# Kernel optimization log

Hardware: AMD Instinct MI355X
Metric: run time of the kernel (lower is better)

The kernel has to match this reference:

```python
import jax, jax.numpy as jnp
import numpy as np

IMG = 1024.0
POOL = 7
STRIDES = (4, 8, 16, 32)  # levels P2..P5
STDS = jnp.array([0.1, 0.1, 0.2, 0.2], dtype=jnp.float32)  # RCNN_TARGET_STDS


def delta2bbox(rois, deltas):
    # rois: [N,4] (y1,x1,y2,x2) pixels; deltas: [N,4]
    d = deltas * STDS  # means are zero
    y1, x1, y2, x2 = rois[:, 0], rois[:, 1], rois[:, 2], rois[:, 3]
    h = y2 - y1
    w = x2 - x1
    cy = y1 + 0.5 * h + d[:, 0] * h
    cx = x1 + 0.5 * w + d[:, 1] * w
    h = h * jnp.exp(d[:, 2])
    w = w * jnp.exp(d[:, 3])
    b = jnp.stack([cy - 0.5 * h, cx - 0.5 * w, cy + 0.5 * h, cx + 0.5 * w], axis=1)
    return jnp.clip(b, 0.0, IMG)


def crop_level(feat, rois, stride):
    # feat: [H,W,C]; bilinear 7x7 crop (crop_and_resize style)
    H, W, _ = feat.shape
    s = rois / stride
    grid = (jnp.arange(POOL, dtype=jnp.float32) + 0.5) / POOL
    ys = s[:, 0:1] + grid[None, :] * (s[:, 2:3] - s[:, 0:1])  # [N,7]
    xs = s[:, 1:2] + grid[None, :] * (s[:, 3:4] - s[:, 1:2])  # [N,7]
    y0f = jnp.clip(jnp.floor(ys), 0.0, H - 1)
    x0f = jnp.clip(jnp.floor(xs), 0.0, W - 1)
    y0 = y0f.astype(jnp.int32)
    x0 = x0f.astype(jnp.int32)
    y1 = jnp.minimum(y0 + 1, H - 1)
    x1 = jnp.minimum(x0 + 1, W - 1)
    wy = jnp.clip(ys - y0f, 0.0, 1.0)[:, :, None, None]  # [N,7,1,1]
    wx = jnp.clip(xs - x0f, 0.0, 1.0)[:, None, :, None]  # [N,1,7,1]
    g = lambda yi, xi: feat[yi[:, :, None], xi[:, None, :]]  # [N,7,7,C]
    return (g(y0, x0) * (1 - wy) * (1 - wx) + g(y0, x1) * (1 - wy) * wx
            + g(y1, x0) * wy * (1 - wx) + g(y1, x1) * wy * wx)


def pyramid_roi_align(feats, rois):
    h = rois[:, 2] - rois[:, 0]
    w = rois[:, 3] - rois[:, 1]
    lvl = jnp.floor(4.0 + jnp.log2(jnp.sqrt(jnp.maximum(h * w, 1e-6)) / 224.0))
    lvl = jnp.clip(lvl, 2.0, 5.0).astype(jnp.int32)
    pooled = 0.0
    for i, (feat, stride) in enumerate(zip(feats, STRIDES)):
        mask = (lvl == i + 2).astype(feat.dtype)[:, None, None, None]
        pooled = pooled + crop_level(feat, rois, stride) * mask
    return pooled  # [N,7,7,C]


def bbox_head(pooled, i, fc1_w, fc1_b, fc2_w, fc2_b, cls_w, cls_b, reg_w, reg_b):
    n = pooled.shape[0]
    x = pooled.reshape(n, -1)
    h1 = jax.nn.relu(x @ fc1_w[i] + fc1_b[i])
    h2 = jax.nn.relu(h1 @ fc2_w[i] + fc2_b[i])
    logits = h2 @ cls_w[i] + cls_b[i]
    probs = jax.nn.softmax(logits, axis=-1)
    deltas = h2 @ reg_w[i] + reg_b[i]
    return logits, probs, deltas


def setup_inputs() -> dict:
    key = jax.random.key(0)
    ks = jax.random.split(key, 16)
    d = {}
    for j, (name, shp) in enumerate([("P2", (1, 256, 256, 256)), ("P3", (1, 128, 128, 256)),
                                     ("P4", (1, 64, 64, 256)), ("P5", (1, 32, 32, 256))]):
        d[name] = jax.random.normal(ks[j], shp, dtype=jnp.float32)
    N = 1000
    u = jax.random.uniform(ks[4], (N, 4))
    hh = 16.0 * 2.0 ** (u[:, 0] * 5.0)  # box sizes 16..512 px, spans all pyramid levels
    ww = 16.0 * 2.0 ** (u[:, 1] * 5.0)
    y1 = u[:, 2] * (IMG - hh)
    x1 = u[:, 3] * (IMG - ww)
    d["rois"] = jnp.stack([y1, x1, y1 + hh, x1 + ww], axis=1)
    d["fc1_w"] = jax.random.normal(ks[5], (3, 12544, 1024), dtype=jnp.float32) * 0.01
    d["fc1_b"] = jnp.zeros((3, 1024), jnp.float32)
    d["fc2_w"] = jax.random.normal(ks[6], (3, 1024, 1024), dtype=jnp.float32) * 0.02
    d["fc2_b"] = jnp.zeros((3, 1024), jnp.float32)
    d["cls_w"] = jax.random.normal(ks[7], (3, 1024, 81), dtype=jnp.float32) * 0.02
    d["cls_b"] = jnp.zeros((3, 81), jnp.float32)
    d["reg_w"] = jax.random.normal(ks[8], (3, 1024, 4), dtype=jnp.float32) * 0.01
    d["reg_b"] = jnp.zeros((3, 4), jnp.float32)
    return d


def reference(P2, P3, P4, P5, rois, fc1_w, fc1_b, fc2_w, fc2_b, cls_w, cls_b, reg_w, reg_b):
    feats = [P2[0], P3[0], P4[0], P5[0]]
    params = (fc1_w, fc1_b, fc2_w, fc2_b, cls_w, cls_b, reg_w, reg_b)
    r = rois
    probs3 = None
    pooled = None
    for i in range(3):
        pooled = pyramid_roi_align(feats, r)
        _, probs3, deltas = bbox_head(pooled, i, *params)
        if i < 2:
            r = delta2bbox(r, deltas)
    # test-time ensemble: heads 1 and 2 re-applied to final pooled regions
    _, probs1, _ = bbox_head(pooled, 0, *params)
    _, probs2, _ = bbox_head(pooled, 1, *params)
    return (probs3 + probs1 + probs2) / 3.0
```

## Files before the change

kernel.cpp:

```cpp
#include <hip/hip_runtime.h>


#define BM 128
#define BN 128
#define BK 32
#define K1 12544
#define MPAD 1024
#define NROI 1000

typedef __bf16 bf16_t;
typedef bf16_t bf16x8 __attribute__((ext_vector_type(8)));
typedef float f32x4 __attribute__((ext_vector_type(4)));
typedef float f32x2 __attribute__((ext_vector_type(2)));
typedef unsigned short u16x4 __attribute__((ext_vector_type(4)));
typedef unsigned short u16x2 __attribute__((ext_vector_type(2)));

__device__ __forceinline__ unsigned short f2bf(float x) {
  unsigned u = __float_as_uint(x);
  return (unsigned short)((u + 0x7fffu + ((u >> 16) & 1u)) >> 16);
}
__device__ __forceinline__ float bf2f(unsigned short h) {
  return __uint_as_float(((unsigned)h) << 16);
}

__device__ __forceinline__ void gld_lds16(const void* g, void* l) {
  __builtin_amdgcn_global_load_lds(
      (__attribute__((address_space(1))) void*)g,
      (__attribute__((address_space(3))) void*)l, 16, 0, 0);
}

template <bool SPLIT>
__global__ __launch_bounds__(256, 4)
void gemm_bf16(const unsigned short* __restrict__ Ah,
               const unsigned short* __restrict__ Al,
               long long strideA_head,
               const unsigned short* __restrict__ Bh,
               const unsigned short* __restrict__ Bl,
               long long strideB_head,
               float* __restrict__ Cpart,
               int Nh, int K, int kcSteps)
{
  __shared__ __align__(16) unsigned short sAh[BM * BK];
  __shared__ __align__(16) unsigned short sBh[BN * BK];
  __shared__ __align__(16) unsigned short sAl[SPLIT ? BM * BK : 8];
  __shared__ __align__(16) unsigned short sBl[SPLIT ? BN * BK : 8];

  const int t = threadIdx.x;
  const int ntile = Nh / BN;
  const int bm = blockIdx.x / ntile;
  const int bn = blockIdx.x % ntile;
  const int s = blockIdx.y;
  const int h = blockIdx.z;
  const int H = gridDim.z;

  const unsigned short* Ab = Ah + (size_t)h * strideA_head + (size_t)bm * BM * K;
  const unsigned short* Bb = Bh + (size_t)h * strideB_head + (size_t)bn * BN * K;
  const unsigned short* Alb = SPLIT ? (Al + (size_t)h * strideA_head + (size_t)bm * BM * K) : (const unsigned short*)0;
  const unsigned short* Blb = SPLIT ? (Bl + (size_t)h * strideB_head + (size_t)bn * BN * K) : (const unsigned short*)0;

  int k0 = s * kcSteps * BK;
  int k1 = min(K, k0 + kcSteps * BK);

  const int srow = t >> 2;
  const int gsw = ((t & 3) ^ ((srow >> 1) & 3)) * 8;
  const int lane = t & 63;
  const int wv = t >> 6;
  const int wm = (wv >> 1) * 64;
  const int wn = (wv & 1) * 64;
  const int lr = lane & 15;
  const int q = lane >> 4;
  const int sw = (lr >> 1) & 3;
  const int cA = (q ^ sw) * 8;

  f32x4 acc[4][4];
  const f32x4 z = {0.f, 0.f, 0.f, 0.f};
#pragma unroll
  for (int i = 0; i < 4; ++i)
#pragma unroll
    for (int j = 0; j < 4; ++j) acc[i][j] = z;

  for (int kk = k0; kk < k1; kk += BK) {
#pragma unroll
    for (int j = 0; j < 2; ++j) {
      int row = j * 64 + srow;
      gld_lds16(Ab + (size_t)row * K + kk + gsw, (char*)sAh + j * 4096 + t * 16);
      gld_lds16(Bb + (size_t)row * K + kk + gsw, (char*)sBh + j * 4096 + t * 16);
      if constexpr (SPLIT) {
        gld_lds16(Alb + (size_t)row * K + kk + gsw, (char*)sAl + j * 4096 + t * 16);
        gld_lds16(Blb + (size_t)row * K + kk + gsw, (char*)sBl + j * 4096 + t * 16);
      }
    }
    __syncthreads();

    bf16x8 af[4], bfr[4];
#pragma unroll
    for (int i = 0; i < 4; ++i) af[i] = *(const bf16x8*)&sAh[(wm + i * 16 + lr) * BK + cA];
#pragma unroll
    for (int j = 0; j < 4; ++j) bfr[j] = *(const bf16x8*)&sBh[(wn + j * 16 + lr) * BK + cA];
#pragma unroll
    for (int i = 0; i < 4; ++i)
#pragma unroll
      for (int j = 0; j < 4; ++j)
        acc[i][j] = __builtin_amdgcn_mfma_f32_16x16x32_bf16(af[i], bfr[j], acc[i][j], 0, 0, 0);

    if constexpr (SPLIT) {
      bf16x8 al[4], bl[4];
#pragma unroll
      for (int i = 0; i < 4; ++i) al[i] = *(const bf16x8*)&sAl[(wm + i * 16 + lr) * BK + cA];
#pragma unroll
      for (int j = 0; j < 4; ++j) bl[j] = *(const bf16x8*)&sBl[(wn + j * 16 + lr) * BK + cA];
#pragma unroll
      for (int i = 0; i < 4; ++i)
#pragma unroll
        for (int j = 0; j < 4; ++j) {
          acc[i][j] = __builtin_amdgcn_mfma_f32_16x16x32_bf16(af[i], bl[j], acc[i][j], 0, 0, 0);
          acc[i][j] = __builtin_amdgcn_mfma_f32_16x16x32_bf16(al[i], bfr[j], acc[i][j], 0, 0, 0);
        }
    }
    __syncthreads();
  }

  float* Cb = Cpart + ((size_t)(s * H + h) * MPAD + (size_t)bm * BM) * Nh + (size_t)bn * BN;
#pragma unroll
  for (int i = 0; i < 4; ++i)
#pragma unroll
    for (int j = 0; j < 4; ++j)
#pragma unroll
      for (int r = 0; r < 4; ++r) {
        int m = wm + i * 16 + q * 4 + r;
        int n = wn + j * 16 + lr;
        Cb[(size_t)m * Nh + n] = acc[i][j][r];
      }
}

#define DS_A(XB, MH) do { \
    rA[0][0]=lda_f(XB,(MH)*4+0,0); rA[0][1]=lda_f(XB,(MH)*4+0,1); \
    rA[1][0]=lda_f(XB,(MH)*4+1,0); rA[1][1]=lda_f(XB,(MH)*4+1,1); \
    rA[2][0]=lda_f(XB,(MH)*4+2,0); rA[2][1]=lda_f(XB,(MH)*4+2,1); \
    rA[3][0]=lda_f(XB,(MH)*4+3,0); rA[3][1]=lda_f(XB,(MH)*4+3,1); } while(0)

#define DS_B(XB, NH) do { \
    rB[(NH)*2+0][0]=ldb_f(XB,(NH)*2+0,0); rB[(NH)*2+0][1]=ldb_f(XB,(NH)*2+0,1); \
    rB[(NH)*2+1][0]=ldb_f(XB,(NH)*2+1,0); rB[(NH)*2+1][1]=ldb_f(XB,(NH)*2+1,1); } while(0)

#define MFMA_Q(MH, NH) do { \
  _Pragma("unroll") \
  for (int ii = 0; ii < 4; ++ii) { \
    _Pragma("unroll") \
    for (int jj = 0; jj < 2; ++jj) { \
      acc[(MH)*4+ii][(NH)*2+jj] = __builtin_amdgcn_mfma_f32_16x16x32_bf16(rA[ii][0], rB[(NH)*2+jj][0], acc[(MH)*4+ii][(NH)*2+jj], 0, 0, 0); \
      acc[(MH)*4+ii][(NH)*2+jj] = __builtin_amdgcn_mfma_f32_16x16x32_bf16(rA[ii][1], rB[(NH)*2+jj][1], acc[(MH)*4+ii][(NH)*2+jj], 0, 0, 0); \
    } } } while(0)

#define PHASE_SYNC() do { \
  __builtin_amdgcn_s_barrier(); \
  asm volatile("s_waitcnt lgkmcnt(0)" ::: "memory"); \
  __builtin_amdgcn_sched_barrier(0); } while(0)

#define PHASE_END() do { \
  __builtin_amdgcn_s_setprio(0); \
  __builtin_amdgcn_s_barrier(); } while(0)

__global__ __launch_bounds__(512, 2)
void gemm256_bf16(const unsigned short* __restrict__ A,
                  const unsigned short* __restrict__ B,
                  float* __restrict__ Cpart,
                  int Ntot, int K, int tilesTotal)
{
  extern __shared__ char lds[];
  const int t = threadIdx.x;
  const int ntile = Ntot >> 8;
  const int bm = blockIdx.x / ntile;
  const int bn = blockIdx.x % ntile;
  const int s = blockIdx.y;
  const int S = gridDim.y;
  const int qp = tilesTotal / S, rp = tilesTotal % S;
  const int t0 = s * qp + (s < rp ? s : rp);
  const int np = qp + (s < rp ? 1 : 0);

  const unsigned short* Ab = A + (size_t)bm * 256 * K;
  const unsigned short* Bb = B + (size_t)bn * 256 * K;

  const int srow = t >> 3;
  const int sgrp = ((t & 7) ^ (srow & 7)) << 3;

  const int lane = t & 63;
  const int wv = t >> 6;
  const int wm = (wv >> 2) << 7;
  const int wn = (wv & 3) << 6;
  const int lr = lane & 15;
  const int q = lane >> 4;

  f32x4 acc[8][4];
  const f32x4 z = {0.f, 0.f, 0.f, 0.f};
#pragma unroll
  for (int i = 0; i < 8; ++i)
#pragma unroll
    for (int j = 0; j < 4; ++j) acc[i][j] = z;

  bf16x8 rA[4][2], rB[4][2];

  auto stage_tile = [&](int xbuf, int kt) {
    const size_t col = ((size_t)(t0 + kt) << 6) + sgrp;
#pragma unroll
    for (int u = 0; u < 4; ++u) {
      const unsigned short* src = (u < 2) ? Ab : Bb;
      const int rbase = ((u & 1) << 7) + srow;
      char* dst = lds + xbuf * 65536 + ((u & 2) << 14) + ((u & 1) << 14) + t * 16;
      gld_lds16(src + (size_t)rbase * K + col, dst);
      gld_lds16(src + (size_t)(rbase + 64) * K + col, dst + 8192);
    }
  };

  auto lda_f = [&](int xbuf, int i, int ks) -> bf16x8 {
    const int row = wm + (i << 4) + lr;
    const int pg = (ks * 4 + q) ^ (row & 7);
    return *(const bf16x8*)(lds + xbuf * 65536 + row * 128 + pg * 16);
  };
  auto ldb_f = [&](int xbuf, int j, int ks) -> bf16x8 {
    const int row = wn + (j << 4) + lr;
    const int pg = (ks * 4 + q) ^ (row & 7);
    return *(const bf16x8*)(lds + xbuf * 65536 + 32768 + row * 128 + pg * 16);
  };

  stage_tile(0, 0);
  if (np > 1) {
    stage_tile(1, 1);
    asm volatile("s_waitcnt vmcnt(8)" ::: "memory");
  } else {
    asm volatile("s_waitcnt vmcnt(0)" ::: "memory");
  }
  __builtin_amdgcn_s_barrier();

  for (int i = 0; i < np; ++i) {
    const int buf = i & 1;
    const bool st = (i + 2 < np);
    DS_A(buf, 0);
    DS_B(buf, 0);
    PHASE_SYNC();
    __builtin_amdgcn_s_setprio(1);
    MFMA_Q(0, 0);
    PHASE_END();
    DS_B(buf, 1);
    PHASE_SYNC();
    __builtin_amdgcn_s_setprio(1);
    MFMA_Q(0, 1);
    PHASE_END();
    DS_A(buf, 1);
    PHASE_SYNC();
    __builtin_amdgcn_s_setprio(1);
    MFMA_Q(1, 0);
    PHASE_END();
    if (st) {
      stage_tile(buf, i + 2);
      asm volatile("s_waitcnt vmcnt(8)" ::: "memory");
    } else {
      asm volatile("s_waitcnt vmcnt(0)" ::: "memory");
    }
    __builtin_amdgcn_s_barrier();
    __builtin_amdgcn_sched_barrier(0);
    __builtin_amdgcn_s_setprio(1);
    MFMA_Q(1, 1);
    __builtin_amdgcn_s_setprio(0);
  }

  float* Cb = Cpart + (size_t)s * MPAD * Ntot +
              (size_t)(bm * 256 + wm) * Ntot + bn * 256 + wn;
#pragma unroll
  for (int i = 0; i < 8; ++i)
#pragma unroll
    for (int j = 0; j < 4; ++j)
#pragma unroll
      for (int r = 0; r < 4; ++r)
        Cb[(size_t)(i * 16 + q * 4 + r) * Ntot + j * 16 + lr] = acc[i][j][r];
}

__global__ __launch_bounds__(256)
void epilogue_kernel(const float* __restrict__ Cpart, int S, int H, int Nh,
                     const float* __restrict__ bias,
                     unsigned short* __restrict__ ohi,
                     unsigned short* __restrict__ olo, int flags)
{
  size_t total = (size_t)H * MPAD * Nh;
  size_t idx = ((size_t)blockIdx.x * 256 + threadIdx.x) * 4;
  if (idx >= total) return;
  int n = (int)(idx % Nh);
  int h = (int)(idx / ((size_t)MPAD * Nh));
  f32x4 v = *(const f32x4*)&bias[(size_t)h * Nh + n];
  for (int s = 0; s < S; ++s) v += *(const f32x4*)&Cpart[(size_t)s * total + idx];
  u16x4 hi, lo;
#pragma unroll
  for (int j = 0; j < 4; ++j) {
    float x = fmaxf(v[j], 0.f);
    hi[j] = f2bf(x);
    lo[j] = f2bf(x - bf2f(hi[j]));
  }
  *(u16x4*)&ohi[idx] = hi;
  if (flags & 4) *(u16x4*)&olo[idx] = lo;
}

__global__ __launch_bounds__(256)
void epilogue_fc1_s2(const float* __restrict__ Cpart, int S,
                     const float* __restrict__ bias,
                     unsigned short* __restrict__ ohi)
{
  const size_t total = (size_t)MPAD * 3072;
  size_t idx = ((size_t)blockIdx.x * 256 + threadIdx.x) * 4;
  if (idx >= total) return;
  int n = (int)(idx % 3072);
  int m = (int)(idx / 3072);
  f32x4 v = *(const f32x4*)&bias[n];
  for (int s = 0; s < S; ++s) v += *(const f32x4*)&Cpart[(size_t)s * total + idx];
  u16x4 hi;
#pragma unroll
  for (int j = 0; j < 4; ++j) hi[j] = f2bf(fmaxf(v[j], 0.f));
  int h = n >> 10;
  *(u16x4*)&ohi[((size_t)h * MPAD + m) * 1024 + (n & 1023)] = hi;
}

__global__ __launch_bounds__(256)
void transpose_convert(const float* __restrict__ W,
                       unsigned short* __restrict__ Thi,
                       unsigned short* __restrict__ Tlo,
                       int K, int N, int loHeads)
{
  __shared__ float tile[32][260];
  int kb = blockIdx.x * 256;
  int nb = blockIdx.y * 32;
  int h = blockIdx.z;
  const float* Wb = W + (size_t)h * K * N + (size_t)kb * N + nb;
  int tn = threadIdx.x & 31;
  int tk = threadIdx.x >> 5;
#pragma unroll
  for (int i = 0; i < 32; ++i) {
    int k = tk + i * 8;
    tile[tn][k] = Wb[(size_t)k * N + tn];
  }
  __syncthreads();
  bool wlo = h < loHeads;
  int l = threadIdx.x & 63;
  int ng = threadIdx.x >> 6;
  size_t ob = (size_t)h * N * K + (size_t)nb * K + kb;
#pragma unroll
  for (int i = 0; i < 8; ++i) {
    int n = ng + i * 4;
    f32x4 v = *(const f32x4*)&tile[n][4 * l];
    u16x4 hi;
#pragma unroll
    for (int j = 0; j < 4; ++j) hi[j] = f2bf(v[j]);
    *(u16x4*)&Thi[ob + (size_t)n * K + 4 * l] = hi;
    if (wlo) {
      u16x4 lo;
#pragma unroll
      for (int j = 0; j < 4; ++j) lo[j] = f2bf(v[j] - bf2f(hi[j]));
      *(u16x4*)&Tlo[ob + (size_t)n * K + 4 * l] = lo;
    }
  }
}

__global__ void transpose_cls(const float* __restrict__ W, unsigned short* __restrict__ T)
{
  int n = blockIdx.x, h = blockIdx.y, t = threadIdx.x;
  size_t ob = ((size_t)h * 128 + n) * 1024;
  if (n < 81) {
    for (int k = t; k < 1024; k += 256)
      T[ob + k] = f2bf(W[((size_t)h * 1024 + k) * 81 + n]);
  } else {
    for (int k = t; k < 1024; k += 256) T[ob + k] = 0;
  }
}

__global__ void roi_align_kernel(const float* __restrict__ rois,
                                 const float* __restrict__ P2, const float* __restrict__ P3,
                                 const float* __restrict__ P4, const float* __restrict__ P5,
                                 unsigned short* __restrict__ phi,
                                 unsigned short* __restrict__ plo, int writeLo)
{
  int m = blockIdx.x;
  int t = threadIdx.x;
  int c = (t & 63) * 4;
  int pg = t >> 6;
  const float* rp = rois + m * 4;
  float y1 = rp[0], x1 = rp[1], y2 = rp[2], x2 = rp[3];
  float hh = y2 - y1, ww = x2 - x1;
  float a = sqrtf(fmaxf(hh * ww, 1e-6f)) / 224.0f;
  float lvl = floorf(4.0f + log2f(a));
  lvl = fminf(fmaxf(lvl, 2.0f), 5.0f);
  int i = (int)lvl - 2;
  const float* f = (i == 0) ? P2 : (i == 1) ? P3 : (i == 2) ? P4 : P5;
  int H = 256 >> i;
  float stride = (float)(4 << i);
  float sy1 = y1 / stride, sx1 = x1 / stride;
  float dy = y2 / stride - sy1, dx = x2 / stride - sx1;
  size_t base = (size_t)m * K1 + c;
  for (int p = pg; p < 49; p += 4) {
    int py = p / 7, px = p % 7;
    float ys = sy1 + ((py + 0.5f) / 7.0f) * dy;
    float xs = sx1 + ((px + 0.5f) / 7.0f) * dx;
    float y0f = fminf(fmaxf(floorf(ys), 0.0f), (float)(H - 1));
    float x0f = fminf(fmaxf(floorf(xs), 0.0f), (float)(H - 1));
    int y0 = (int)y0f, x0 = (int)x0f;
    int y1i = min(y0 + 1, H - 1), x1i = min(x0 + 1, H - 1);
    float wy = fminf(fmaxf(ys - y0f, 0.0f), 1.0f);
    float wx = fminf(fmaxf(xs - x0f, 0.0f), 1.0f);
    f32x4 v00 = *(const f32x4*)(f + ((size_t)y0 * H + x0) * 256 + c);
    f32x4 v01 = *(const f32x4*)(f + ((size_t)y0 * H + x1i) * 256 + c);
    f32x4 v10 = *(const f32x4*)(f + ((size_t)y1i * H + x0) * 256 + c);
    f32x4 v11 = *(const f32x4*)(f + ((size_t)y1i * H + x1i) * 256 + c);
    float w00 = (1.f - wy) * (1.f - wx), w01 = (1.f - wy) * wx;
    float w10 = wy * (1.f - wx), w11 = wy * wx;
    f32x4 v = v00 * w00 + v01 * w01 + v10 * w10 + v11 * w11;
    u16x4 hi;
#pragma unroll
    for (int j = 0; j < 4; ++j) hi[j] = f2bf(v[j]);
    *(u16x4*)&phi[base + p * 256] = hi;
    if (writeLo) {
      u16x4 lo;
#pragma unroll
      for (int j = 0; j < 4; ++j) lo[j] = f2bf(v[j] - bf2f(hi[j]));
      *(u16x2*)&plo[base + p * 256] = *(u16x2*)&lo;
      *(u16x2*)&plo[base + p * 256 + 2] = *((u16x2*)&lo + 1);
    }
  }
}

__global__ void reg_delta_kernel(const float* __restrict__ Cpart, int S,
                                 const float* __restrict__ fb,
                                 const float* __restrict__ rw, const float* __restrict__ rb,
                                 const float* __restrict__ rin, float* __restrict__ rout)
{
  int m = blockIdx.x, t = threadIdx.x;
  float s0 = 0, s1 = 0, s2 = 0, s3 = 0;
  for (int n = t; n < 1024; n += 256) {
    float v = fb[n];
    for (int s = 0; s < S; ++s) v += Cpart[((size_t)s * 1024 + m) * 1024 + n];
    v = fmaxf(v, 0.f);
    const float* w = rw + (size_t)n * 4;
    s0 += v * w[0]; s1 += v * w[1]; s2 += v * w[2]; s3 += v * w[3];
  }
#pragma unroll
  for (int o = 32; o > 0; o >>= 1) {
    s0 += __shfl_xor(s0, o, 64);
    s1 += __shfl_xor(s1, o, 64);
    s2 += __shfl_xor(s2, o, 64);
    s3 += __shfl_xor(s3, o, 64);
  }
  __shared__ float part[4][4];
  int w = t >> 6;
  if ((t & 63) == 0) { part[w][0] = s0; part[w][1] = s1; part[w][2] = s2; part[w][3] = s3; }
  __syncthreads();
  if (t == 0) {
    float d0 = (part[0][0] + part[1][0] + part[2][0] + part[3][0] + rb[0]) * 0.1f;
    float d1 = (part[0][1] + part[1][1] + part[2][1] + part[3][1] + rb[1]) * 0.1f;
    float d2 = (part[0][2] + part[1][2] + part[2][2] + part[3][2] + rb[2]) * 0.2f;
    float d3 = (part[0][3] + part[1][3] + part[2][3] + part[3][3] + rb[3]) * 0.2f;
    const float* r = rin + m * 4;
    float y1 = r[0], x1 = r[1], y2 = r[2], x2 = r[3];
    float h = y2 - y1, wd = x2 - x1;
    float cy = y1 + 0.5f * h + d0 * h;
    float cx = x1 + 0.5f * wd + d1 * wd;
    float nh = h * expf(d2);
    float nw = wd * expf(d3);
    float* ro = rout + m * 4;
    ro[0] = fminf(fmaxf(cy - 0.5f * nh, 0.f), 1024.f);
    ro[1] = fminf(fmaxf(cx - 0.5f * nw, 0.f), 1024.f);
    ro[2] = fminf(fmaxf(cy + 0.5f * nh, 0.f), 1024.f);
    ro[3] = fminf(fmaxf(cx + 0.5f * nw, 0.f), 1024.f);
  }
}

__global__ void softmax_avg_kernel(const float* __restrict__ Cpart, int S,
                                   const float* __restrict__ cls_b,
                                   float* __restrict__ out)
{
  int m = blockIdx.x, t = threadIdx.x;
  __shared__ float sh[128];
  float pacc = 0.0f;
  for (int h = 0; h < 3; ++h) {
    float x = -3.0e38f;
    if (t < 81) {
      x = cls_b[h * 81 + t];
      for (int s = 0; s < S; ++s)
        x += Cpart[((size_t)(s * 3 + h) * 1024 + m) * 128 + t];
    }
    sh[t] = x; __syncthreads();
    for (int o = 64; o > 0; o >>= 1) { if (t < o) sh[t] = fmaxf(sh[t], sh[t + o]); __syncthreads(); }
    float mx = sh[0]; __syncthreads();
    float e = (t < 81) ? expf(x - mx) : 0.0f;
    sh[t] = e; __syncthreads();
    for (int o = 64; o > 0; o >>= 1) { if (t < o) sh[t] += sh[t + o]; __syncthreads(); }
    float sum = sh[0]; __syncthreads();
    pacc += e / sum;
  }
  if (t < 81) out[(size_t)m * 81 + t] = pacc / 3.0f;
}

extern "C" void kernel_launch(void* const* d_in, const int* in_sizes, int n_in,
                              void* d_out, int out_size, void* d_ws, size_t ws_size,
                              hipStream_t stream)
{
  const float* P2 = (const float*)d_in[0];
  const float* P3 = (const float*)d_in[1];
  const float* P4 = (const float*)d_in[2];
  const float* P5 = (const float*)d_in[3];
  const float* rois = (const float*)d_in[4];
  const float* fc1_w = (const float*)d_in[5];
  const float* fc1_b = (const float*)d_in[6];
  const float* fc2_w = (const float*)d_in[7];
  const float* fc2_b = (const float*)d_in[8];
  const float* cls_w = (const float*)d_in[9];
  const float* cls_b = (const float*)d_in[10];
  const float* reg_w = (const float*)d_in[11];
  const float* reg_b = (const float*)d_in[12];
  float* out = (float*)d_out;

  char* ws = (char*)d_ws;
  size_t off = 0;
  auto alloc = [&](size_t b) -> char* {
    char* p = ws + off;
    off = (off + b + 255) & ~(size_t)255;
    return p;
  };
  unsigned short* w1t_hi = (unsigned short*)alloc(3ull * 1024 * K1 * 2);
  unsigned short* w2t_hi = (unsigned short*)alloc(3ull * 1024 * 1024 * 2);
  unsigned short* w2t_lo = (unsigned short*)alloc(2ull * 1024 * 1024 * 2);
  unsigned short* w3t    = (unsigned short*)alloc(3ull * 128 * 1024 * 2);
  unsigned short* phi    = (unsigned short*)alloc((size_t)MPAD * K1 * 2);
  unsigned short* plo    = (unsigned short*)alloc((size_t)MPAD * K1 * 2);
  unsigned short* h1_hi  = (unsigned short*)alloc(3ull * MPAD * 1024 * 2);
  unsigned short* h1_lo  = (unsigned short*)alloc((size_t)MPAD * 1024 * 2);
  unsigned short* h2_hi  = (unsigned short*)alloc(3ull * MPAD * 1024 * 2);
  float* r1              = (float*)alloc(16384);
  float* r2              = (float*)alloc(16384);
  const size_t w1lo_bytes = 2ull * 1024 * K1 * 2;
  unsigned short* w1t_lo = (unsigned short*)alloc(w1lo_bytes);

  const size_t SLAB = (size_t)MPAD * 1024 * 4;
  size_t tail = (ws_size > off) ? (ws_size - off) : 0;

  int S01 = (int)(tail / SLAB);
  if (S01 > 8) S01 = 8;
  if (S01 < 1) S01 = 1;
  float* cpart01 = (float*)(ws + off);
  const int S2 = 4;
  float* cpart2 = (float*)w1t_lo;

  const int fc1Steps01 = (392 + S01 - 1) / S01;
  const int fc2Steps01 = (32 + S01 - 1) / S01;

  const long long hs1 = (long long)1024 * K1;
  const long long hs2 = (long long)1024 * 1024;

  dim3 b256(256);

  hipLaunchKernelGGL(transpose_convert, dim3(K1 / 256, 32, 3), b256, 0, stream,
                     fc1_w, w1t_hi, w1t_lo, K1, 1024, 2);
  hipLaunchKernelGGL(transpose_convert, dim3(4, 32, 3), b256, 0, stream,
                     fc2_w, w2t_hi, w2t_lo, 1024, 1024, 2);
  hipLaunchKernelGGL(transpose_cls, dim3(128, 3), b256, 0, stream, cls_w, w3t);
  hipMemsetAsync(phi + (size_t)NROI * K1, 0, (size_t)(MPAD - NROI) * K1 * 2, stream);
  hipMemsetAsync(plo + (size_t)NROI * K1, 0, (size_t)(MPAD - NROI) * K1 * 2, stream);

  for (int st = 0; st < 2; ++st) {
    const float* rin = (st == 0) ? rois : r1;
    float* rout = (st == 0) ? r1 : r2;
    hipLaunchKernelGGL(roi_align_kernel, dim3(NROI), b256, 0, stream,
                       rin, P2, P3, P4, P5, phi, plo, 1);
    hipLaunchKernelGGL((gemm_bf16<true>), dim3(64, S01, 1), b256, 0, stream,
                       phi, plo, 0LL,
                       w1t_hi + (size_t)st * hs1, w1t_lo + (size_t)st * hs1, 0LL,
                       cpart01, 1024, K1, fc1Steps01);
    hipLaunchKernelGGL(epilogue_kernel, dim3(1024), b256, 0, stream,
                       cpart01, S01, 1, 1024, fc1_b + st * 1024,
                       h1_hi, h1_lo, 4);
    hipLaunchKernelGGL((gemm_bf16<true>), dim3(64, S01, 1), b256, 0, stream,
                       h1_hi, h1_lo, 0LL,
                       w2t_hi + (size_t)st * hs2, w2t_lo + (size_t)st * hs2, 0LL,
                       cpart01, 1024, 1024, fc2Steps01);
    hipLaunchKernelGGL(reg_delta_kernel, dim3(NROI), b256, 0, stream,
                       cpart01, S01, fc2_b + st * 1024,
                       reg_w + (size_t)st * 1024 * 4, reg_b + st * 4,
                       rin, rout);
  }

  hipLaunchKernelGGL(roi_align_kernel, dim3(NROI), b256, 0, stream,
                     r2, P2, P3, P4, P5, phi, plo, 0);
  {
    const size_t SLAB3 = (size_t)MPAD * 3072 * 4;
    size_t availC2 = ws_size - (size_t)((char*)w1t_lo - ws);
    int S2f = 5;
    while (S2f > 1 && (size_t)S2f * SLAB3 > availC2) --S2f;
    hipLaunchKernelGGL(gemm256_bf16, dim3(48, S2f), dim3(512), 131072, stream,
                       phi, w1t_hi, cpart2, 3072, K1, 196);
    hipLaunchKernelGGL(epilogue_fc1_s2, dim3(3072), b256, 0, stream,
                       cpart2, S2f, fc1_b, h1_hi);
  }
  hipLaunchKernelGGL((gemm_bf16<false>), dim3(64, S2, 3), b256, 0, stream,
                     h1_hi, (const unsigned short*)0, hs2,
                     w2t_hi, (const unsigned short*)0, hs2,
                     cpart2, 1024, 1024, (32 + S2 - 1) / S2);
  hipLaunchKernelGGL(epilogue_kernel, dim3(3072), b256, 0, stream,
                     cpart2, S2, 3, 1024, fc2_b,
                     h2_hi, (unsigned short*)0, 0);
  hipLaunchKernelGGL((gemm_bf16<false>), dim3(8, 8, 3), b256, 0, stream,
                     h2_hi, (const unsigned short*)0, hs2,
                     w3t, (const unsigned short*)0, (long long)128 * 1024,
                     cpart2, 128, 1024, 4);
  hipLaunchKernelGGL(softmax_avg_kernel, dim3(NROI), dim3(128), 0, stream,
                     cpart2, 8, cls_b, out);
}
```

Measured before the change: 824.4 us.

## Add 128x256 split-precision GEMM kernel with LDS double-buffering for FC1 stages

Introduces gemm256s_bf16, a 512-thread kernel with 128x256 tiles that keeps the hi/lo bf16 split (three MFMAs per product) and double-buffers hi/lo A and B tiles in 96KB of LDS via direct global-to-LDS loads, using phased barriers and priority hints. It replaces the 128x128 split GEMM for the two refinement-stage FC1 layers. The aim is more operand reuse per byte loaded and better MFMA/load overlap on the dominant K=12544 GEMM. The costs are higher LDS usage per block, which limits occupancy, and fewer tiles per split, which could leave some CUs underused.

Result: faster. 789.3 us (-4.3%).

```diff
diff --git a/kernel.cpp b/kernel.cpp
--- a/kernel.cpp
+++ b/kernel.cpp
@@ -28,6 +28,15 @@
       (__attribute__((address_space(1))) void*)g,
       (__attribute__((address_space(3))) void*)l, 16, 0, 0);
 }
+
+#define PHASE_SYNC() do { \
+  __builtin_amdgcn_s_barrier(); \
+  asm volatile("s_waitcnt lgkmcnt(0)" ::: "memory"); \
+  __builtin_amdgcn_sched_barrier(0); } while(0)
+
+#define PHASE_END() do { \
+  __builtin_amdgcn_s_setprio(0); \
+  __builtin_amdgcn_s_barrier(); } while(0)
 
 template <bool SPLIT>
 __global__ __launch_bounds__(256, 4)
@@ -151,15 +160,6 @@
       acc[(MH)*4+ii][(NH)*2+jj] = __builtin_amdgcn_mfma_f32_16x16x32_bf16(rA[ii][0], rB[(NH)*2+jj][0], acc[(MH)*4+ii][(NH)*2+jj], 0, 0, 0); \
       acc[(MH)*4+ii][(NH)*2+jj] = __builtin_amdgcn_mfma_f32_16x16x32_bf16(rA[ii][1], rB[(NH)*2+jj][1], acc[(MH)*4+ii][(NH)*2+jj], 0, 0, 0); \
     } } } while(0)
-
-#define PHASE_SYNC() do { \
-  __builtin_amdgcn_s_barrier(); \
-  asm volatile("s_waitcnt lgkmcnt(0)" ::: "memory"); \
-  __builtin_amdgcn_sched_barrier(0); } while(0)
-
-#define PHASE_END() do { \
-  __builtin_amdgcn_s_setprio(0); \
-  __builtin_amdgcn_s_barrier(); } while(0)
 
 __global__ __launch_bounds__(512, 2)
 void gemm256_bf16(const unsigned short* __restrict__ A,
@@ -268,6 +268,142 @@
               (size_t)(bm * 256 + wm) * Ntot + bn * 256 + wn;
 #pragma unroll
   for (int i = 0; i < 8; ++i)
+#pragma unroll
+    for (int j = 0; j < 4; ++j)
+#pragma unroll
+      for (int r = 0; r < 4; ++r)
+        Cb[(size_t)(i * 16 + q * 4 + r) * Ntot + j * 16 + lr] = acc[i][j][r];
+}
+
+#define S_DS_A(XB, MH) do { \
+    rAh[0]=s_lda(XB,0,(MH)*2+0); rAh[1]=s_lda(XB,0,(MH)*2+1); \
+    rAl[0]=s_lda(XB,1,(MH)*2+0); rAl[1]=s_lda(XB,1,(MH)*2+1); } while(0)
+
+#define S_DS_B(XB, NH) do { \
+    rBh[(NH)*2+0]=s_ldb(XB,0,(NH)*2+0); rBh[(NH)*2+1]=s_ldb(XB,0,(NH)*2+1); \
+    rBl[(NH)*2+0]=s_ldb(XB,1,(NH)*2+0); rBl[(NH)*2+1]=s_ldb(XB,1,(NH)*2+1); } while(0)
+
+#define S_MFMA_Q(MH, NH) do { \
+  _Pragma("unroll") \
+  for (int ii = 0; ii < 2; ++ii) { \
+    _Pragma("unroll") \
+    for (int jj = 0; jj < 2; ++jj) { \
+      f32x4* a = &acc[(MH)*2+ii][(NH)*2+jj]; \
+      *a = __builtin_amdgcn_mfma_f32_16x16x32_bf16(rAh[ii], rBh[(NH)*2+jj], *a, 0, 0, 0); \
+      *a = __builtin_amdgcn_mfma_f32_16x16x32_bf16(rAh[ii], rBl[(NH)*2+jj], *a, 0, 0, 0); \
+      *a = __builtin_amdgcn_mfma_f32_16x16x32_bf16(rAl[ii], rBh[(NH)*2+jj], *a, 0, 0, 0); \
+    } } } while(0)
+
+__global__ __launch_bounds__(512, 2)
+void gemm256s_bf16(const unsigned short* __restrict__ Ah,
+                   const unsigned short* __restrict__ Al,
+                   const unsigned short* __restrict__ Bh,
+                   const unsigned short* __restrict__ Bl,
+                   float* __restrict__ Cpart,
+                   int Ntot, int K, int tilesTotal)
+{
+  extern __shared__ char lds[];
+  const int t = threadIdx.x;
+  const int ntile = Ntot >> 8;
+  const int bm = blockIdx.x / ntile;
+  const int bn = blockIdx.x % ntile;
+  const int s = blockIdx.y;
+  const int S = gridDim.y;
+  const int qp = tilesTotal / S, rp = tilesTotal % S;
+  const int t0 = s * qp + (s < rp ? s : rp);
+  const int np = qp + (s < rp ? 1 : 0);
+
+  const unsigned short* Ahb = Ah + (size_t)bm * 128 * K;
+  const unsigned short* Alb = Al + (size_t)bm * 128 * K;
+  const unsigned short* Bhb = Bh + (size_t)bn * 256 * K;
+  const unsigned short* Blb = Bl + (size_t)bn * 256 * K;
+
+  const int srow = t >> 2;
+  const int sgrp = ((t & 3) ^ (srow & 3)) << 3;
+
+  const int lane = t & 63;
+  const int wv = t >> 6;
+  const int wm = (wv >> 2) << 6;
+  const int wn = (wv & 3) << 6;
+  const int lr = lane & 15;
+  const int q = lane >> 4;
+
+  f32x4 acc[4][4];
+  const f32x4 z = {0.f, 0.f, 0.f, 0.f};
+#pragma unroll
+  for (int i = 0; i < 4; ++i)
+#pragma unroll
+    for (int j = 0; j < 4; ++j) acc[i][j] = z;
+
+  bf16x8 rAh[2], rAl[2], rBh[4], rBl[4];
+
+  auto stage_tile = [&](int xbuf, int kt) {
+    const size_t col = ((size_t)(t0 + kt) << 5) + sgrp;
+    char* base = lds + xbuf * 49152;
+    gld_lds16(Ahb + (size_t)srow * K + col, base + t * 16);
+    gld_lds16(Alb + (size_t)srow * K + col, base + 8192 + t * 16);
+    gld_lds16(Bhb + (size_t)srow * K + col, base + 16384 + t * 16);
+    gld_lds16(Bhb + (size_t)(srow + 128) * K + col, base + 16384 + 8192 + t * 16);
+    gld_lds16(Blb + (size_t)srow * K + col, base + 32768 + t * 16);
+    gld_lds16(Blb + (size_t)(srow + 128) * K + col, base + 32768 + 8192 + t * 16);
+  };
+
+  auto s_lda = [&](int xbuf, int pl, int i) -> bf16x8 {
+    const int row = wm + (i << 4) + lr;
+    const int pg = q ^ (row & 3);
+    return *(const bf16x8*)(lds + xbuf * 49152 + pl * 8192 + row * 64 + pg * 16);
+  };
+  auto s_ldb = [&](int xbuf, int pl, int j) -> bf16x8 {
+    const int row = wn + (j << 4) + lr;
+    const int pg = q ^ (row & 3);
+    return *(const bf16x8*)(lds + xbuf * 49152 + 16384 + pl * 16384 + row * 64 + pg * 16);
+  };
+
+  stage_tile(0, 0);
+  if (np > 1) {
+    stage_tile(1, 1);
+    asm volatile("s_waitcnt vmcnt(6)" ::: "memory");
+  } else {
+    asm volatile("s_waitcnt vmcnt(0)" ::: "memory");
+  }
+  __builtin_amdgcn_s_barrier();
+
+  for (int i = 0; i < np; ++i) {
+    const int buf = i & 1;
+    const bool st = (i + 2 < np);
+    S_DS_A(buf, 0);
+    S_DS_B(buf, 0);
+    PHASE_SYNC();
+    __builtin_amdgcn_s_setprio(1);
+    S_MFMA_Q(0, 0);
+    PHASE_END();
+    S_DS_B(buf, 1);
+    PHASE_SYNC();
+    __builtin_amdgcn_s_setprio(1);
+    S_MFMA_Q(0, 1);
+    PHASE_END();
+    S_DS_A(buf, 1);
+    PHASE_SYNC();
+    __builtin_amdgcn_s_setprio(1);
+    S_MFMA_Q(1, 0);
+    PHASE_END();
+    if (st) {
+      stage_tile(buf, i + 2);
+      asm volatile("s_waitcnt vmcnt(6)" ::: "memory");
+    } else {
+      asm volatile("s_waitcnt vmcnt(0)" ::: "memory");
+    }
+    __builtin_amdgcn_s_barrier();
+    __builtin_amdgcn_sched_barrier(0);
+    __builtin_amdgcn_s_setprio(1);
+    S_MFMA_Q(1, 1);
+    __builtin_amdgcn_s_setprio(0);
+  }
+
+  float* Cb = Cpart + (size_t)s * MPAD * Ntot +
+              (size_t)(bm * 128 + wm) * Ntot + bn * 256 + wn;
+#pragma unroll
+  for (int i = 0; i < 4; ++i)
 #pragma unroll
     for (int j = 0; j < 4; ++j)
 #pragma unroll
@@ -545,7 +681,6 @@
   const int S2 = 4;
   float* cpart2 = (float*)w1t_lo;
 
-  const int fc1Steps01 = (392 + S01 - 1) / S01;
   const int fc2Steps01 = (32 + S01 - 1) / S01;
 
   const long long hs1 = (long long)1024 * K1;
@@ -566,10 +701,10 @@
     float* rout = (st == 0) ? r1 : r2;
     hipLaunchKernelGGL(roi_align_kernel, dim3(NROI), b256, 0, stream,
                        rin, P2, P3, P4, P5, phi, plo, 1);
-    hipLaunchKernelGGL((gemm_bf16<true>), dim3(64, S01, 1), b256, 0, stream,
-                       phi, plo, 0LL,
-                       w1t_hi + (size_t)st * hs1, w1t_lo + (size_t)st * hs1, 0LL,
-                       cpart01, 1024, K1, fc1Steps01);
+    hipLaunchKernelGGL(gemm256s_bf16, dim3(32, S01), dim3(512), 98304, stream,
+                       phi, plo,
+                       w1t_hi + (size_t)st * hs1, w1t_lo + (size_t)st * hs1,
+                       cpart01, 1024, K1, 392);
     hipLaunchKernelGGL(epilogue_kernel, dim3(1024), b256, 0, stream,
                        cpart01, S01, 1, 1024, fc1_b + st * 1024,
                        h1_hi, h1_lo, 4);
```
